# Performance work log

Hardware: AMD Instinct MI355X
Metric: run time of the kernel (lower is better)

The kernel has to match this reference:

```python
import jax, jax.numpy as jnp
import numpy as np

N = 5000      # nodes
E = 80000     # edges (avg degree 16)
B = 8         # batch of graph signals sharing one graph
IN = 30       # input feature dim (10 steps x 3)
H = 4         # attention heads
D = 64        # hidden dim per head
HD = H * D    # 256
OUT = 3       # output features per step
NUM_GAT_LAYERS = 4  # num_layer=5 -> 1 + (5-2) layers
EPS = 1e-5


def setup_inputs() -> dict:
    key = jax.random.key(0)
    ks = jax.random.split(key, 40)
    inp = {}
    inp["xx"] = jax.random.normal(ks[0], (B, N, IN), dtype=jnp.float32)
    inp["src"] = jax.random.randint(ks[1], (E,), 0, N, dtype=jnp.int32)
    inp["dst"] = jax.random.randint(ks[2], (E,), 0, N, dtype=jnp.int32)
    dims = [IN, HD, HD, HD]
    k = 3
    for l in range(NUM_GAT_LAYERS):
        fan_in = dims[l]
        inp[f"W{l}"] = jax.random.normal(ks[k], (fan_in, HD), dtype=jnp.float32) / np.sqrt(fan_in); k += 1
        inp[f"al{l}"] = jax.random.normal(ks[k], (H, D), dtype=jnp.float32) * 0.1; k += 1
        inp[f"ar{l}"] = jax.random.normal(ks[k], (H, D), dtype=jnp.float32) * 0.1; k += 1
        inp[f"gamma{l}"] = jnp.ones((HD,), dtype=jnp.float32)
        inp[f"beta{l}"] = jnp.zeros((HD,), dtype=jnp.float32)
    inp["W_out"] = jax.random.normal(ks[k], (HD, OUT), dtype=jnp.float32) / np.sqrt(HD); k += 1
    inp["b_out"] = jnp.zeros((OUT,), dtype=jnp.float32)
    inp["output_length"] = 5
    return inp


def _gat_conv(x, W, al, ar, src, dst):
    # DGL GATConv: fc -> per-head attn logits -> edge softmax over dst -> scatter-sum
    h = (x @ W).reshape(N, H, D)                       # [N,H,D]
    el = (h * al).sum(-1)                              # [N,H]
    er = (h * ar).sum(-1)                              # [N,H]
    e = jax.nn.leaky_relu(el[src] + er[dst], 0.2)      # [E,H]
    m = jax.ops.segment_max(e, dst, num_segments=N)    # [N,H] (stable softmax)
    ex = jnp.exp(e - m[dst])                           # [E,H]
    s = jax.ops.segment_sum(ex, dst, num_segments=N)   # [N,H]
    alpha = ex / s[dst]                                # [E,H]
    return jax.ops.segment_sum(alpha[:, :, None] * h[src], dst, num_segments=N)  # [N,H,D]


def _gat_layer(x, W, al, ar, gamma, beta, src, dst):
    # per-sample GATConv, flatten heads, BatchNorm1d (training stats) over (B,N), LeakyReLU
    out = jax.vmap(lambda xb: _gat_conv(xb, W, al, ar, src, dst))(x)  # [B,N,H,D]
    out = out.reshape(B, N, HD)
    mu = out.mean(axis=(0, 1))
    var = out.var(axis=(0, 1))  # biased, matches torch BN normalization
    out = (out - mu) * jax.lax.rsqrt(var + EPS) * gamma + beta
    return jax.nn.leaky_relu(out, 0.01)


def reference(xx, src, dst,
              W0, al0, ar0, gamma0, beta0,
              W1, al1, ar1, gamma1, beta1,
              W2, al2, ar2, gamma2, beta2,
              W3, al3, ar3, gamma3, beta3,
              W_out, b_out, output_length):
    layers = [(W0, al0, ar0, gamma0, beta0),
              (W1, al1, ar1, gamma1, beta1),
              (W2, al2, ar2, gamma2, beta2),
              (W3, al3, ar3, gamma3, beta3)]
    outputs = []
    for _ in range(output_length):
        h = xx
        for (W, al, ar, g, b) in layers:
            h = _gat_layer(h, W, al, ar, g, b, src, dst)
        out = h @ W_out + b_out                      # [B,N,OUT]
        xx = jnp.concatenate([xx[:, :, 3:], out], axis=-1)
        outputs.append(out[:, :, None, :])
    return jnp.concatenate(outputs, axis=2)          # [B,N,T,OUT]
```

## Files before the change

kernel.cpp:

```cpp
#include <hip/hip_runtime.h>
#include <math.h>

#define NNODES 5000
#define NEDGES 80000
#define NB 8
#define NIN 30
#define K0PAD 32
#define NH 4
#define ND 64
#define NHD 256
#define NT 5
#define NOUT 3
#define ROWS (NB * NNODES)
#define BNEPS 1e-5f
#define KP 40
#define NREP 64
#define BM 32

#define GLOBAL_AS __attribute__((address_space(1)))
#define LDS_AS __attribute__((address_space(3)))

typedef short shortx8 __attribute__((ext_vector_type(8)));
typedef _Float16 halfx8 __attribute__((ext_vector_type(8)));
typedef _Float16 halfx4 __attribute__((ext_vector_type(4)));
typedef _Float16 halfx2 __attribute__((ext_vector_type(2)));
typedef float floatx4 __attribute__((ext_vector_type(4)));

static __device__ __forceinline__ unsigned short f2h(float f) {
    union { _Float16 h; unsigned short u; } v;
    v.h = (_Float16)f;
    return v.u;
}
static __device__ __forceinline__ float h2f(unsigned short u) {
    union { _Float16 h; unsigned short u; } v;
    v.u = u;
    return (float)v.h;
}


__global__ void count_kernel(const int* __restrict__ dst, int* __restrict__ counts, int n) {
    int e = blockIdx.x * blockDim.x + threadIdx.x;
    if (e < n) atomicAdd(&counts[dst[e]], 1);
}

__global__ __launch_bounds__(1024) void scan_kernel(const int* __restrict__ counts,
                                                    int* __restrict__ offsets, int n) {
    __shared__ int smem[1024];
    const int CH = 5;
    int tid = threadIdx.x;
    int base = tid * CH;
    int loc[CH];
    int s = 0;
    for (int j = 0; j < CH; ++j) {
        int i = base + j;
        int v = (i < n) ? counts[i] : 0;
        loc[j] = s;
        s += v;
    }
    smem[tid] = s;
    __syncthreads();
    for (int off = 1; off < 1024; off <<= 1) {
        int v = (tid >= off) ? smem[tid - off] : 0;
        __syncthreads();
        smem[tid] += v;
        __syncthreads();
    }
    int excl = smem[tid] - s;
    for (int j = 0; j < CH; ++j) {
        int i = base + j;
        if (i < n) offsets[i] = excl + loc[j];
    }
    if (tid == 1023) offsets[n] = smem[1023];
}

__global__ void fill_kernel(const int* __restrict__ src, const int* __restrict__ dst,
                            const int* __restrict__ offsets, int* __restrict__ cursor,
                            int* __restrict__ csr_src, int n) {
    int e = blockIdx.x * blockDim.x + threadIdx.x;
    if (e >= n) return;
    int d = dst[e];
    int pos = offsets[d] + atomicAdd(&cursor[d], 1);
    csr_src[pos] = src[e];
}


__global__ void pack_xx_kernel(const float* __restrict__ xx, unsigned short* __restrict__ xx16) {
    int idx = blockIdx.x * blockDim.x + threadIdx.x;
    if (idx >= ROWS * K0PAD) return;
    int g = idx >> 5;
    int k = idx & 31;
    float v = (k < NIN) ? xx[(size_t)g * NIN + k] : 0.0f;
    xx16[idx] = f2h(v);
}

__global__ void packWt_kernel(const float* __restrict__ W0, const float* __restrict__ W1,
                              const float* __restrict__ W2, const float* __restrict__ W3,
                              unsigned short* __restrict__ P0, unsigned short* __restrict__ P1,
                              unsigned short* __restrict__ P2, unsigned short* __restrict__ P3) {
    int l = blockIdx.y;
    const float* W = (l == 0) ? W0 : (l == 1) ? W1 : (l == 2) ? W2 : W3;
    unsigned short* WtP = (l == 0) ? P0 : (l == 1) ? P1 : (l == 2) ? P2 : P3;
    int Kin = (l == 0) ? NIN : NHD;
    int Kpad = (l == 0) ? K0PAD : NHD;
    int n = blockIdx.x;
    int k = threadIdx.x;
    if (k < Kpad) {
        float v = (k < Kin) ? W[(size_t)k * NHD + n] : 0.0f;
        int t = k >> 5;
        int quad = (k >> 3) & 3;
        int j = k & 7;
        int p = n * 4 + (quad ^ ((n >> 1) & 3));
        WtP[(size_t)t * (NHD * 32) + p * 8 + j] = f2h(v);
    }
}


__global__ __launch_bounds__(256) void gemm_mfma_kernel(
    const unsigned short* __restrict__ A, const unsigned short* __restrict__ Wt,
    const float* __restrict__ alw, const float* __restrict__ arw,
    const float* __restrict__ sums_read, float* __restrict__ sums_zero,
    const float* __restrict__ gamma, const float* __restrict__ beta, int apply_bn,
    unsigned short* __restrict__ C16, float* __restrict__ el, float* __restrict__ er,
    int K) {
    __shared__ __align__(16) short As[BM * KP];
    __shared__ __align__(16) short Bs[256 * 32];
    __shared__ float bn_scale[NHD];
    __shared__ float bn_shift[NHD];
    int tid = threadIdx.x;
    {
        int zi = blockIdx.x * 256 + tid;
        if (zi < NREP * 2 * NHD) sums_zero[zi] = 0.0f;
    }
    if (apply_bn) {
        int c = tid;
        float s = 0.0f, s2 = 0.0f;
        for (int r2 = 0; r2 < NREP; ++r2) {
            s += sums_read[r2 * 2 * NHD + c];
            s2 += sums_read[r2 * 2 * NHD + NHD + c];
        }
        const float invn = 1.0f / (float)ROWS;
        float mu = s * invn;
        float var = s2 * invn - mu * mu;
        float sc = rsqrtf(var + BNEPS) * gamma[c];
        bn_scale[c] = sc;
        bn_shift[c] = beta[c] - mu * sc;
    }
    __syncthreads();

    int wave = tid >> 6;
    int lane = tid & 63;
    int c = lane & 15;
    int quad = lane >> 4;
    int xorv = (c >> 1) & 3;
    int row0 = blockIdx.x * BM;

    floatx4 acc[2][4];
#pragma unroll
    for (int mt = 0; mt < 2; ++mt)
#pragma unroll
        for (int nt = 0; nt < 4; ++nt) acc[mt][nt] = (floatx4){0.f, 0.f, 0.f, 0.f};

    int r = tid >> 2;
    int seg = tid & 3;
    for (int k0 = 0; k0 < K; k0 += 32) {
        const unsigned short* gB = Wt + (size_t)(k0 >> 5) * (NHD * 32);
#pragma unroll
        for (int i = 0; i < 4; ++i) {
            int ci = i * 256 + tid;
            __builtin_amdgcn_global_load_lds(
                (const GLOBAL_AS unsigned int*)(gB + ci * 8),
                (LDS_AS unsigned int*)(&Bs[ci * 8]), 16, 0, 0);
        }
        if (r < BM) {
            shortx8 v = *(const shortx8*)(A + (size_t)(row0 + r) * K + k0 + seg * 8);
            if (apply_bn) {
                halfx8 hv = *(halfx8*)&v;
                int kg = k0 + seg * 8;
#pragma unroll
                for (int j = 0; j < 8; ++j) {
                    float x = (float)hv[j];
                    x = fmaf(x, bn_scale[kg + j], bn_shift[kg + j]);
                    x = (x > 0.0f) ? x : 0.01f * x;
                    hv[j] = (_Float16)x;
                }
                v = *(shortx8*)&hv;
            }
            *(shortx8*)(&As[r * KP + seg * 8]) = v;
        }
        __syncthreads();
        halfx8 a[2], b[4];
#pragma unroll
        for (int mt = 0; mt < 2; ++mt)
            a[mt] = *(const halfx8*)(&As[(mt * 16 + c) * KP + quad * 8]);
#pragma unroll
        for (int nt = 0; nt < 4; ++nt) {
            int pq = (wave * 64 + nt * 16 + c) * 4 + (quad ^ xorv);
            b[nt] = *(const halfx8*)(&Bs[pq * 8]);
        }
#pragma unroll
        for (int mt = 0; mt < 2; ++mt)
#pragma unroll
            for (int nt = 0; nt < 4; ++nt)
                acc[mt][nt] = __builtin_amdgcn_mfma_f32_16x16x32_f16(a[mt], b[nt],
                                                                     acc[mt][nt], 0, 0, 0);
        __syncthreads();
    }

    float alv[4], arv[4];
#pragma unroll
    for (int nt = 0; nt < 4; ++nt) {
        alv[nt] = alw[wave * 64 + nt * 16 + c];
        arv[nt] = arw[wave * 64 + nt * 16 + c];
    }
#pragma unroll
    for (int mt = 0; mt < 2; ++mt) {
#pragma unroll
        for (int rr = 0; rr < 4; ++rr) {
            int row = row0 + mt * 16 + quad * 4 + rr;
            float pl = 0.0f, pr = 0.0f;
#pragma unroll
            for (int nt = 0; nt < 4; ++nt) {
                float v = acc[mt][nt][rr];
                C16[(size_t)row * NHD + wave * 64 + nt * 16 + c] = f2h(v);
                pl += v * alv[nt];
                pr += v * arv[nt];
            }
#pragma unroll
            for (int o = 1; o < 16; o <<= 1) {
                pl += __shfl_xor(pl, o);
                pr += __shfl_xor(pr, o);
            }
            if (c == mt * 4 + rr) {
                el[(size_t)row * NH + wave] = pl;
                er[(size_t)row * NH + wave] = pr;
            }
        }
    }
}


__global__ __launch_bounds__(256) void attn_kernel(const unsigned short* __restrict__ h16,
                                                   const float* __restrict__ el,
                                                   const float* __restrict__ er,
                                                   const int* __restrict__ offsets,
                                                   const int* __restrict__ csr_src,
                                                   unsigned short* __restrict__ out16,
                                                   float* __restrict__ sums_cur) {
    __shared__ float bnpart[4][2][NHD];
    int p = blockIdx.x;
    int tid = threadIdx.x;
    int b = p & 7;
    int wave = tid >> 6;
    int lane = tid & 63;
    int head = lane >> 4;
    int li = lane & 15;
    int n = ((p >> 3) << 2) + wave;
    int g = b * NNODES + n;
    int start = offsets[n];
    int deg = offsets[n + 1] - start;
    const float* elb = el + (size_t)b * NNODES * NH;
    float er_nh = er[(size_t)g * NH + head];
    float* bw = &bnpart[wave][0][0];

    if (deg == 0) {
        *(unsigned long long*)(out16 + (size_t)g * NHD + lane * 4) = 0ULL;
        int c4 = lane * 4;
#pragma unroll
        for (int j = 0; j < 4; ++j) {
            bw[c4 + j] = 0.0f;
            bw[NHD + c4 + j] = 0.0f;
        }
    } else if (deg <= 64) {
        float e[4], w[4];
        int s[4];
#pragma unroll
        for (int k = 0; k < 4; ++k) {
            int idx = k * 16 + li;
            if (idx < deg) {
                s[k] = csr_src[start + idx];
                float t = elb[s[k] * NH + head] + er_nh;
                e[k] = (t > 0.0f) ? t : 0.2f * t;
            } else {
                s[k] = 0;
                e[k] = -INFINITY;
            }
        }
        float mx = fmaxf(fmaxf(e[0], e[1]), fmaxf(e[2], e[3]));
#pragma unroll
        for (int o = 8; o; o >>= 1) mx = fmaxf(mx, __shfl_xor(mx, o));
        float sm = 0.0f;
#pragma unroll
        for (int k = 0; k < 4; ++k) {
            w[k] = __expf(e[k] - mx);
            sm += w[k];
        }
#pragma unroll
        for (int o = 8; o; o >>= 1) sm += __shfl_xor(sm, o);

        int sub = lane >> 5;
        int i32 = lane & 31;
        int hsel = (lane & 24) << 1;
        float smh = __shfl(sm, hsel);
        const unsigned short* hrow = h16 + (size_t)b * NNODES * NHD + i32 * 8;
        float a0 = 0.f, a1 = 0.f, a2 = 0.f, a3 = 0.f;
        float a4 = 0.f, a5 = 0.f, a6 = 0.f, a7 = 0.f;
#define GATHER_CHUNK(K)                                                          \
        if (deg > (K) * 16) {                                                    \
            int cnt = deg - (K) * 16;                                            \
            cnt = (cnt > 16) ? 16 : cnt;                                         \
            int j = 0;                                                           \
            for (; j + 4 <= cnt; j += 4) {                                       \
                int sa = __shfl(s[K], j + sub);                                  \
                float wa = __shfl(w[K], hsel + j + sub);                         \
                int sb = __shfl(s[K], j + 2 + sub);                              \
                float wb = __shfl(w[K], hsel + j + 2 + sub);                     \
                halfx8 ha = *(const halfx8*)(hrow + (size_t)sa * NHD);           \
                halfx8 hb = *(const halfx8*)(hrow + (size_t)sb * NHD);           \
                a0 += wa * (float)ha[0]; a1 += wa * (float)ha[1];                \
                a2 += wa * (float)ha[2]; a3 += wa * (float)ha[3];                \
                a4 += wa * (float)ha[4]; a5 += wa * (float)ha[5];                \
                a6 += wa * (float)ha[6]; a7 += wa * (float)ha[7];                \
                a0 += wb * (float)hb[0]; a1 += wb * (float)hb[1];                \
                a2 += wb * (float)hb[2]; a3 += wb * (float)hb[3];                \
                a4 += wb * (float)hb[4]; a5 += wb * (float)hb[5];                \
                a6 += wb * (float)hb[6]; a7 += wb * (float)hb[7];                \
            }                                                                    \
            for (; j < cnt; j += 2) {                                            \
                int e2 = j + sub;                                                \
                bool valid = (e2 < cnt);                                         \
                int ec = valid ? e2 : (cnt - 1);                                 \
                int sa = __shfl(s[K], ec);                                       \
                float wa0 = __shfl(w[K], hsel + ec);                             \
                float wa = valid ? wa0 : 0.0f;                                   \
                halfx8 ha = *(const halfx8*)(hrow + (size_t)sa * NHD);           \
                a0 += wa * (float)ha[0]; a1 += wa * (float)ha[1];                \
                a2 += wa * (float)ha[2]; a3 += wa * (float)ha[3];                \
                a4 += wa * (float)ha[4]; a5 += wa * (float)ha[5];                \
                a6 += wa * (float)ha[6]; a7 += wa * (float)ha[7];                \
            }                                                                    \
        }
        GATHER_CHUNK(0)
        GATHER_CHUNK(1)
        GATHER_CHUNK(2)
        GATHER_CHUNK(3)
#undef GATHER_CHUNK
        a0 += __shfl_xor(a0, 32); a1 += __shfl_xor(a1, 32);
        a2 += __shfl_xor(a2, 32); a3 += __shfl_xor(a3, 32);
        a4 += __shfl_xor(a4, 32); a5 += __shfl_xor(a5, 32);
        a6 += __shfl_xor(a6, 32); a7 += __shfl_xor(a7, 32);
        if (sub == 0) {
            float inv = 1.0f / smh;
            halfx8 o8;
            o8[0] = (_Float16)(a0 * inv); o8[1] = (_Float16)(a1 * inv);
            o8[2] = (_Float16)(a2 * inv); o8[3] = (_Float16)(a3 * inv);
            o8[4] = (_Float16)(a4 * inv); o8[5] = (_Float16)(a5 * inv);
            o8[6] = (_Float16)(a6 * inv); o8[7] = (_Float16)(a7 * inv);
            *(halfx8*)(out16 + (size_t)g * NHD + i32 * 8) = o8;
            int c8 = i32 * 8;
#pragma unroll
            for (int j = 0; j < 8; ++j) {
                float v = (float)o8[j];
                bw[c8 + j] = v;
                bw[NHD + c8 + j] = v * v;
            }
        }
    } else {
        const unsigned short* hbase = h16 + (size_t)b * NNODES * NHD + lane * 4;
        float mx = -INFINITY;
        for (int i = li; i < deg; i += 16) {
            int s2 = csr_src[start + i];
            float t = elb[s2 * NH + head] + er_nh;
            t = (t > 0.0f) ? t : 0.2f * t;
            mx = fmaxf(mx, t);
        }
#pragma unroll
        for (int o = 8; o; o >>= 1) mx = fmaxf(mx, __shfl_xor(mx, o));
        float sm = 0.0f;
        for (int i = li; i < deg; i += 16) {
            int s2 = csr_src[start + i];
            float t = elb[s2 * NH + head] + er_nh;
            t = (t > 0.0f) ? t : 0.2f * t;
            sm += __expf(t - mx);
        }
#pragma unroll
        for (int o = 8; o; o >>= 1) sm += __shfl_xor(sm, o);
        float a0 = 0.f, a1 = 0.f, a2 = 0.f, a3 = 0.f;
        for (int j = 0; j < deg; ++j) {
            int s2 = csr_src[start + j];
            float t = elb[s2 * NH + head] + er_nh;
            t = (t > 0.0f) ? t : 0.2f * t;
            float wj = __expf(t - mx);
            halfx4 hv = *(const halfx4*)(hbase + (size_t)s2 * NHD);
            a0 += wj * (float)hv[0];
            a1 += wj * (float)hv[1];
            a2 += wj * (float)hv[2];
            a3 += wj * (float)hv[3];
        }
        float inv = 1.0f / sm;
        halfx4 o4;
        o4[0] = (_Float16)(a0 * inv);
        o4[1] = (_Float16)(a1 * inv);
        o4[2] = (_Float16)(a2 * inv);
        o4[3] = (_Float16)(a3 * inv);
        *(halfx4*)(out16 + (size_t)g * NHD + lane * 4) = o4;
        int c4 = lane * 4;
#pragma unroll
        for (int j = 0; j < 4; ++j) {
            float v = (float)o4[j];
            bw[c4 + j] = v;
            bw[NHD + c4 + j] = v * v;
        }
    }
    __syncthreads();
    {
        int c = tid;
        float s = bnpart[0][0][c] + bnpart[1][0][c] + bnpart[2][0][c] + bnpart[3][0][c];
        float s2 = bnpart[0][1][c] + bnpart[1][1][c] + bnpart[2][1][c] + bnpart[3][1][c];
        float* sr = sums_cur + (p & (NREP - 1)) * 2 * NHD;
        atomicAdd(&sr[c], s);
        atomicAdd(&sr[NHD + c], s2);
    }
}


__global__ __launch_bounds__(256) void headout_kernel(const unsigned short* __restrict__ x16,
                                                      const float* __restrict__ sums,
                                                      const float* __restrict__ gamma,
                                                      const float* __restrict__ beta,
                                                      const float* __restrict__ Wout,
                                                      const float* __restrict__ bout,
                                                      float* __restrict__ out,
                                                      unsigned short* __restrict__ xx16, int t) {
    __shared__ float bsc[NHD];
    __shared__ float bsh[NHD];
    {
        int c = threadIdx.x;
        float s = 0.0f, s2 = 0.0f;
        for (int r2 = 0; r2 < NREP; ++r2) {
            s += sums[r2 * 2 * NHD + c];
            s2 += sums[r2 * 2 * NHD + NHD + c];
        }
        const float invn = 1.0f / (float)ROWS;
        float mu = s * invn;
        float var = s2 * invn - mu * mu;
        float sc = rsqrtf(var + BNEPS) * gamma[c];
        bsc[c] = sc;
        bsh[c] = beta[c] - mu * sc;
    }
    __syncthreads();

    int wave = threadIdx.x >> 6;
    int lane = threadIdx.x & 63;
    int g = blockIdx.x * 4 + wave;
    int c0 = lane * 4;
    halfx4 hv = *(const halfx4*)(x16 + (size_t)g * NHD + c0);
    float vv[4];
#pragma unroll
    for (int j = 0; j < 4; ++j) {
        float x = fmaf((float)hv[j], bsc[c0 + j], bsh[c0 + j]);
        vv[j] = (x > 0.0f) ? x : 0.01f * x;
    }
    float r0 = vv[0] * Wout[(c0 + 0) * NOUT + 0] + vv[1] * Wout[(c0 + 1) * NOUT + 0] +
               vv[2] * Wout[(c0 + 2) * NOUT + 0] + vv[3] * Wout[(c0 + 3) * NOUT + 0];
    float r1 = vv[0] * Wout[(c0 + 0) * NOUT + 1] + vv[1] * Wout[(c0 + 1) * NOUT + 1] +
               vv[2] * Wout[(c0 + 2) * NOUT + 1] + vv[3] * Wout[(c0 + 3) * NOUT + 1];
    float r2 = vv[0] * Wout[(c0 + 0) * NOUT + 2] + vv[1] * Wout[(c0 + 1) * NOUT + 2] +
               vv[2] * Wout[(c0 + 2) * NOUT + 2] + vv[3] * Wout[(c0 + 3) * NOUT + 2];
#pragma unroll
    for (int o = 32; o; o >>= 1) {
        r0 += __shfl_xor(r0, o);
        r1 += __shfl_xor(r1, o);
        r2 += __shfl_xor(r2, o);
    }
    float o0 = r0 + bout[0], o1 = r1 + bout[1], o2 = r2 + bout[2];
    if (lane == 0) {
        float* op = out + ((size_t)g * NT + t) * NOUT;
        op[0] = o0;
        op[1] = o1;
        op[2] = o2;
    }
    float oldv = (lane < NIN) ? h2f(xx16[(size_t)g * K0PAD + lane]) : 0.0f;
    float shifted = __shfl(oldv, lane + 3);
    float newv = (lane < 27) ? shifted : (lane == 27 ? o0 : (lane == 28 ? o1 : o2));
    if (lane < NIN) xx16[(size_t)g * K0PAD + lane] = f2h(newv);
}


extern "C" void kernel_launch(void* const* d_in, const int* in_sizes, int n_in,
                              void* d_out, int out_size, void* d_ws, size_t ws_size,
                              hipStream_t stream) {
    const float* xx = (const float*)d_in[0];
    const int* src = (const int*)d_in[1];
    const int* dst = (const int*)d_in[2];
    const float* W[4] = {(const float*)d_in[3], (const float*)d_in[8],
                         (const float*)d_in[13], (const float*)d_in[18]};
    const float* al[4] = {(const float*)d_in[4], (const float*)d_in[9],
                          (const float*)d_in[14], (const float*)d_in[19]};
    const float* ar[4] = {(const float*)d_in[5], (const float*)d_in[10],
                          (const float*)d_in[15], (const float*)d_in[20]};
    const float* gamma[4] = {(const float*)d_in[6], (const float*)d_in[11],
                             (const float*)d_in[16], (const float*)d_in[21]};
    const float* beta[4] = {(const float*)d_in[7], (const float*)d_in[12],
                            (const float*)d_in[17], (const float*)d_in[22]};
    const float* W_out = (const float*)d_in[23];
    const float* b_out = (const float*)d_in[24];
    float* out = (float*)d_out;

    float* wsf = (float*)d_ws;
    float* el = wsf;
    float* er = el + (size_t)ROWS * NH;
    float* sumsA = er + (size_t)ROWS * NH;
    float* sumsB = sumsA + NREP * 2 * NHD;
    unsigned short* h16 = (unsigned short*)(sumsB + NREP * 2 * NHD);
    unsigned short* act16 = h16 + (size_t)ROWS * NHD;
    unsigned short* xx16 = act16 + (size_t)ROWS * NHD;
    unsigned short* Wt0 = xx16 + (size_t)ROWS * K0PAD;
    unsigned short* Wt1 = Wt0 + 256 * K0PAD;
    unsigned short* Wt2 = Wt1 + 256 * NHD;
    unsigned short* Wt3 = Wt2 + 256 * NHD;
    int* counts = (int*)(Wt3 + 256 * NHD);
    int* offsets = counts + NNODES;
    int* cursor = offsets + NNODES + 8;
    int* csr_src = cursor + NNODES;
    const unsigned short* Wt[4] = {Wt0, Wt1, Wt2, Wt3};

    hipMemsetAsync(counts, 0, NNODES * sizeof(int), stream);
    count_kernel<<<(NEDGES + 255) / 256, 256, 0, stream>>>(dst, counts, NEDGES);
    scan_kernel<<<1, 1024, 0, stream>>>(counts, offsets, NNODES);
    hipMemsetAsync(cursor, 0, NNODES * sizeof(int), stream);
    fill_kernel<<<(NEDGES + 255) / 256, 256, 0, stream>>>(src, dst, offsets, cursor,
                                                          csr_src, NEDGES);
    pack_xx_kernel<<<(ROWS * K0PAD + 255) / 256, 256, 0, stream>>>(xx, xx16);
    packWt_kernel<<<dim3(256, 4), 256, 0, stream>>>(W[0], W[1], W[2], W[3],
                                                    (unsigned short*)Wt0,
                                                    (unsigned short*)Wt1,
                                                    (unsigned short*)Wt2,
                                                    (unsigned short*)Wt3);

    int idx = 0;
    for (int t = 0; t < NT; ++t) {
        for (int l = 0; l < 4; ++l) {
            const unsigned short* A16 = (l == 0) ? xx16 : act16;
            int K = (l == 0) ? K0PAD : NHD;
            int apply_bn = (l > 0) ? 1 : 0;
            const float* pg = gamma[(l > 0) ? l - 1 : 0];
            const float* pb = beta[(l > 0) ? l - 1 : 0];
            float* cur = (idx & 1) ? sumsB : sumsA;
            const float* prev = (idx & 1) ? sumsA : sumsB;
            gemm_mfma_kernel<<<ROWS / BM, 256, 0, stream>>>(A16, Wt[l], al[l], ar[l],
                                                            prev, cur, pg, pb, apply_bn,
                                                            h16, el, er, K);
            attn_kernel<<<ROWS / 4, 256, 0, stream>>>(h16, el, er, offsets, csr_src,
                                                      act16, cur);
            ++idx;
        }
        headout_kernel<<<ROWS / 4, 256, 0, stream>>>(act16, sumsB, gamma[3], beta[3],
                                                     W_out, b_out, out, xx16, t);
    }
}
```

Baseline: 1.527 ms.

## Compute BatchNorm scale/shift once per layer in a dedicated kernel

Adds a single-block kernel that reduces the replicated BN partial sums once per layer, writes the per-channel scale and shift, and zeroes the sums in place. The GEMM and head-output kernels then only load the 512 precomputed floats instead of every block re-reducing 64 replicas of partial sums. This removes heavy redundant global/L2 reads in every block, at the cost of one extra tiny kernel launch per layer and a serialized single-block step.

New measurement: 1.336 ms. 1.14x faster.

```diff
diff --git a/kernel.cpp b/kernel.cpp
--- a/kernel.cpp
+++ b/kernel.cpp
@@ -115,11 +115,32 @@
 }
 
 
+__global__ __launch_bounds__(256) void bnfinal_kernel(float* __restrict__ sums,
+                                                      const float* __restrict__ gamma,
+                                                      const float* __restrict__ beta,
+                                                      float* __restrict__ bnss) {
+    int c = threadIdx.x;
+    float s = 0.0f, s2 = 0.0f;
+#pragma unroll
+    for (int r = 0; r < NREP; ++r) {
+        s += sums[r * 2 * NHD + c];
+        s2 += sums[r * 2 * NHD + NHD + c];
+        sums[r * 2 * NHD + c] = 0.0f;
+        sums[r * 2 * NHD + NHD + c] = 0.0f;
+    }
+    const float invn = 1.0f / (float)ROWS;
+    float mu = s * invn;
+    float var = s2 * invn - mu * mu;
+    float sc = rsqrtf(var + BNEPS) * gamma[c];
+    bnss[c] = sc;
+    bnss[NHD + c] = beta[c] - mu * sc;
+}
+
+
 __global__ __launch_bounds__(256) void gemm_mfma_kernel(
     const unsigned short* __restrict__ A, const unsigned short* __restrict__ Wt,
     const float* __restrict__ alw, const float* __restrict__ arw,
-    const float* __restrict__ sums_read, float* __restrict__ sums_zero,
-    const float* __restrict__ gamma, const float* __restrict__ beta, int apply_bn,
+    const float* __restrict__ bnss, int apply_bn,
     unsigned short* __restrict__ C16, float* __restrict__ el, float* __restrict__ er,
     int K) {
     __shared__ __align__(16) short As[BM * KP];
@@ -127,23 +148,9 @@
     __shared__ float bn_scale[NHD];
     __shared__ float bn_shift[NHD];
     int tid = threadIdx.x;
-    {
-        int zi = blockIdx.x * 256 + tid;
-        if (zi < NREP * 2 * NHD) sums_zero[zi] = 0.0f;
-    }
     if (apply_bn) {
-        int c = tid;
-        float s = 0.0f, s2 = 0.0f;
-        for (int r2 = 0; r2 < NREP; ++r2) {
-            s += sums_read[r2 * 2 * NHD + c];
-            s2 += sums_read[r2 * 2 * NHD + NHD + c];
-        }
-        const float invn = 1.0f / (float)ROWS;
-        float mu = s * invn;
-        float var = s2 * invn - mu * mu;
-        float sc = rsqrtf(var + BNEPS) * gamma[c];
-        bn_scale[c] = sc;
-        bn_shift[c] = beta[c] - mu * sc;
+        bn_scale[tid] = bnss[tid];
+        bn_shift[tid] = bnss[NHD + tid];
     }
     __syncthreads();
 
@@ -424,9 +431,7 @@
 
 
 __global__ __launch_bounds__(256) void headout_kernel(const unsigned short* __restrict__ x16,
-                                                      const float* __restrict__ sums,
-                                                      const float* __restrict__ gamma,
-                                                      const float* __restrict__ beta,
+                                                      const float* __restrict__ bnss,
                                                       const float* __restrict__ Wout,
                                                       const float* __restrict__ bout,
                                                       float* __restrict__ out,
@@ -435,17 +440,8 @@
     __shared__ float bsh[NHD];
     {
         int c = threadIdx.x;
-        float s = 0.0f, s2 = 0.0f;
-        for (int r2 = 0; r2 < NREP; ++r2) {
-            s += sums[r2 * 2 * NHD + c];
-            s2 += sums[r2 * 2 * NHD + NHD + c];
-        }
-        const float invn = 1.0f / (float)ROWS;
-        float mu = s * invn;
-        float var = s2 * invn - mu * mu;
-        float sc = rsqrtf(var + BNEPS) * gamma[c];
-        bsc[c] = sc;
-        bsh[c] = beta[c] - mu * sc;
+        bsc[c] = bnss[c];
+        bsh[c] = bnss[NHD + c];
     }
     __syncthreads();
 
@@ -509,9 +505,9 @@
     float* wsf = (float*)d_ws;
     float* el = wsf;
     float* er = el + (size_t)ROWS * NH;
-    float* sumsA = er + (size_t)ROWS * NH;
-    float* sumsB = sumsA + NREP * 2 * NHD;
-    unsigned short* h16 = (unsigned short*)(sumsB + NREP * 2 * NHD);
+    float* sums = er + (size_t)ROWS * NH;
+    float* bnss = sums + NREP * 2 * NHD;
+    unsigned short* h16 = (unsigned short*)(bnss + 2 * NHD);
     unsigned short* act16 = h16 + (size_t)ROWS * NHD;
     unsigned short* xx16 = act16 + (size_t)ROWS * NHD;
     unsigned short* Wt0 = xx16 + (size_t)ROWS * K0PAD;
@@ -525,6 +521,7 @@
     const unsigned short* Wt[4] = {Wt0, Wt1, Wt2, Wt3};
 
     hipMemsetAsync(counts, 0, NNODES * sizeof(int), stream);
+    hipMemsetAsync(sums, 0, NREP * 2 * NHD * sizeof(float), stream);
     count_kernel<<<(NEDGES + 255) / 256, 256, 0, stream>>>(dst, counts, NEDGES);
     scan_kernel<<<1, 1024, 0, stream>>>(counts, offsets, NNODES);
     hipMemsetAsync(cursor, 0, NNODES * sizeof(int), stream);
@@ -537,24 +534,19 @@
                                                     (unsigned short*)Wt2,
                                                     (unsigned short*)Wt3);
 
-    int idx = 0;
     for (int t = 0; t < NT; ++t) {
         for (int l = 0; l < 4; ++l) {
             const unsigned short* A16 = (l == 0) ? xx16 : act16;
             int K = (l == 0) ? K0PAD : NHD;
             int apply_bn = (l > 0) ? 1 : 0;
-            const float* pg = gamma[(l > 0) ? l - 1 : 0];
-            const float* pb = beta[(l > 0) ? l - 1 : 0];
-            float* cur = (idx & 1) ? sumsB : sumsA;
-            const float* prev = (idx & 1) ? sumsA : sumsB;
             gemm_mfma_kernel<<<ROWS / BM, 256, 0, stream>>>(A16, Wt[l], al[l], ar[l],
-                                                            prev, cur, pg, pb, apply_bn,
+                                                            bnss, apply_bn,
                                                             h16, el, er, K);
             attn_kernel<<<ROWS / 4, 256, 0, stream>>>(h16, el, er, offsets, csr_src,
-                                                      act16, cur);
-            ++idx;
-        }
-        headout_kernel<<<ROWS / 4, 256, 0, stream>>>(act16, sumsB, gamma[3], beta[3],
-                                                     W_out, b_out, out, xx16, t);
-    }
-}
+                                                      act16, sums);
+            bnfinal_kernel<<<1, 256, 0, stream>>>(sums, gamma[l], beta[l], bnss);
+        }
+        headout_kernel<<<ROWS / 4, 256, 0, stream>>>(act16, bnss, W_out, b_out,
+                                                     out, xx16, t);
+    }
+}
```
